# Kernel tuning notes

Hardware: AMD Instinct MI355X
Metric: run time of the kernel (lower is better)

## Reference

```python
import jax, jax.numpy as jnp
import numpy as np

N = 10000
H_INPUTS = 128
H = 512
RW_LEN = 16
BATCH = 512


def setup_inputs() -> dict:
    key = jax.random.key(0)
    ks = jax.random.split(key, 5)
    x = jax.random.normal(ks[0], (BATCH, RW_LEN, N + 1), dtype=jnp.float32)
    # xavier-ish scaled params
    W_down = jax.random.normal(ks[1], (N, H_INPUTS), dtype=jnp.float32) * (1.0 / np.sqrt(N))
    W_cell = jax.random.normal(ks[2], (H_INPUTS + 1 + H, 4 * H), dtype=jnp.float32) * (1.0 / np.sqrt(H_INPUTS + 1 + H))
    b_cell = jnp.zeros((4 * H,), dtype=jnp.float32)
    W_out = jax.random.normal(ks[3], (H, 1), dtype=jnp.float32) * (1.0 / np.sqrt(H))
    b_out = jnp.zeros((1,), dtype=jnp.float32)
    return {"x": x, "W_down": W_down, "W_cell": W_cell, "b_cell": b_cell,
            "W_out": W_out, "b_out": b_out}


def _forward(x, W_down, W_cell, b_cell, W_out, b_out):
    B = x.shape[0]
    x_rw = x[:, :, :N]                       # [B, T, N]
    x_weights = x[:, :, -1:]                 # [B, T, 1]
    xa = jnp.einsum('btn,nh->bth', x_rw, W_down)  # down-projection [B, T, H_in]
    xc = jnp.concatenate([xa, x_weights], axis=2)  # [B, T, H_in+1]
    xc_t = jnp.swapaxes(xc, 0, 1)            # [T, B, H_in+1] for scan

    h0 = jnp.zeros((B, H), dtype=x.dtype)
    c0 = jnp.zeros((B, H), dtype=x.dtype)

    def step(carry, xt):
        h, c = carry
        gates = jnp.concatenate([xt, h], axis=1) @ W_cell + b_cell  # [B, 4H]
        i_g, c_g, f_g, o_g = jnp.split(gates, 4, axis=1)
        # custom forget-gate bias of +1
        c_new = c * jax.nn.sigmoid(f_g + 1.0) + jax.nn.sigmoid(i_g) * jnp.tanh(c_g)
        h_new = jax.nn.sigmoid(o_g) * jnp.tanh(c_new)
        return (h_new, c_new), None

    (h, _), _ = jax.lax.scan(step, (h0, c0), xc_t)
    pred = h @ W_out + b_out                 # [B, 1]
    return pred


def reference(x, W_down, W_cell, b_cell, W_out, b_out):
    return _forward(x, W_down, W_cell, b_cell, W_out, b_out)
```

## Files before the change

kernel.cpp:

```cpp
#include <hip/hip_runtime.h>
#include <cmath>

#define TID ((int)threadIdx.x)

typedef __bf16 bf16_t;
typedef bf16_t bf16x8 __attribute__((ext_vector_type(8)));
typedef float floatx4 __attribute__((ext_vector_type(4)));

#define MFMA(a, b, c) __builtin_amdgcn_mfma_f32_16x16x32_bf16(a, b, c, 0, 0, 0)
#define WAIT_BAR(N)  do { asm volatile("s_waitcnt vmcnt(" #N ")" ::: "memory"); \
                          __builtin_amdgcn_s_barrier(); \
                          __builtin_amdgcn_sched_barrier(0); } while (0)
#define LGKM_BAR     do { asm volatile("s_waitcnt lgkmcnt(0)" ::: "memory"); \
                          __builtin_amdgcn_s_barrier(); \
                          __builtin_amdgcn_sched_barrier(0); } while (0)

constexpr int N_IN = 10000;
constexpr int XP   = 10001;
constexpr int KPD  = 10240;
constexpr int HH   = 512;
constexpr int TT   = 16;
constexpr int NB   = 512;
constexpr int MROW = 8192;
constexpr int KSPLIT = 16;
constexpr int KCHUNK = 640;
constexpr int KT_A = 10;

__device__ __forceinline__ float sigm(float x) { return 1.0f / (1.0f + expf(-x)); }

__device__ __forceinline__ void gload16(const void* g, void* lds) {
  __builtin_amdgcn_global_load_lds(
      (const __attribute__((address_space(1))) unsigned int*)g,
      (__attribute__((address_space(3))) unsigned int*)lds, 16, 0, 0);
}

__global__ __launch_bounds__(256)
void kPrepWd(const float* __restrict__ Wd, bf16_t* __restrict__ Whi, bf16_t* __restrict__ Wlo) {
  __shared__ float Ts[64][133];
  const int k0 = blockIdx.x * 64;
  #pragma unroll
  for (int i = 0; i < 32; ++i) {
    int f = TID + 256 * i;
    int kk = f >> 7, c = f & 127;
    int k = k0 + kk;
    Ts[kk][c] = (k < N_IN) ? Wd[(size_t)k * 128 + c] : 0.0f;
  }
  __syncthreads();
  const int lane = TID & 63, w = TID >> 6;
  for (int pass = 0; pass < 32; ++pass) {
    int c = pass * 4 + w;
    float v = Ts[lane][c];
    bf16_t hi = (bf16_t)v;
    bf16_t lo = (bf16_t)(v - (float)hi);
    Whi[(size_t)c * KPD + k0 + lane] = hi;
    Wlo[(size_t)c * KPD + k0 + lane] = lo;
  }
}

__global__ __launch_bounds__(256)
void kPrepWc(const float* __restrict__ Wc, bf16_t* __restrict__ Wxh, bf16_t* __restrict__ Wxl,
             float* __restrict__ wN, bf16_t* __restrict__ Whh, bf16_t* __restrict__ Whl) {
  __shared__ float Ts[64][133];
  const int k0 = blockIdx.x * 64;
  const int c0 = blockIdx.y * 128;
  #pragma unroll
  for (int i = 0; i < 32; ++i) {
    int f = TID + 256 * i;
    int kk = f >> 7, cc = f & 127;
    int k = k0 + kk;
    Ts[kk][cc] = (k < 641) ? Wc[(size_t)k * 2048 + c0 + cc] : 0.0f;
  }
  __syncthreads();
  const int lane = TID & 63, w = TID >> 6;
  const int k = k0 + lane;
  for (int pass = 0; pass < 32; ++pass) {
    int cc = pass * 4 + w;
    int c = c0 + cc;
    float v = Ts[lane][cc];
    bf16_t hi = (bf16_t)v;
    bf16_t lo = (bf16_t)(v - (float)hi);
    if (k < 128) {
      Wxh[(size_t)c * 128 + k] = hi;
      Wxl[(size_t)c * 128 + k] = lo;
    } else if (k == 128) {
      wN[c] = v;
    } else if (k < 641) {
      Whh[(size_t)c * 512 + (k - 129)] = hi;
      Whl[(size_t)c * 512 + (k - 129)] = lo;
    }
  }
}

__global__ __launch_bounds__(256, 2)
void kA_mfma(const float* __restrict__ x, const bf16_t* __restrict__ Whi,
             const bf16_t* __restrict__ Wlo, float* __restrict__ parts) {
  __shared__ __align__(16) bf16_t Bt[2][2048 * 8];
  const int lane = TID & 63, w = TID >> 6;
  const int row0 = blockIdx.x * 128 + w * 32;
  const int kbase = blockIdx.y * KCHUNK;
  floatx4 acc[2][8] = {};

  auto STAGE = [&](int buf, int kt) {
    const int k0 = kbase + kt * 64;
    #pragma unroll
    for (int i = 0; i < 8; ++i) {
      int L = i * 256 + TID;
      int arr = L >> 10, col = (L >> 3) & 127, g = L & 7;
      int gs = g ^ (col & 7);
      const bf16_t* src = (arr ? Wlo : Whi) + (size_t)col * KPD + k0 + gs * 8;
      gload16(src, &Bt[buf][(size_t)L * 8]);
    }
  };
  auto LOADX = [&](float4 (&xb)[2][2][2], int kt) {
    const int k0 = kbase + kt * 64;
    #pragma unroll
    for (int rf = 0; rf < 2; ++rf) {
      const float* xp = x + (size_t)(row0 + rf * 16 + (lane & 15)) * XP;
      #pragma unroll
      for (int h = 0; h < 2; ++h) {
        int kk0 = k0 + h * 32 + (lane >> 4) * 8;
        int kc = (kk0 < N_IN) ? kk0 : (N_IN - 8);
        float4 v0 = *(const float4*)(xp + kc);
        float4 v1 = *(const float4*)(xp + kc + 4);
        if (kk0 >= N_IN) {
          v0 = make_float4(0.f, 0.f, 0.f, 0.f);
          v1 = make_float4(0.f, 0.f, 0.f, 0.f);
        }
        xb[rf][h][0] = v0;
        xb[rf][h][1] = v1;
      }
    }
  };
  auto COMPUTE = [&](int buf, const float4 (&xb)[2][2][2]) {
    #pragma unroll
    for (int h = 0; h < 2; ++h) {
      const int p = h * 4 + (lane >> 4);
      bf16x8 ahi[2], alo[2];
      #pragma unroll
      for (int rf = 0; rf < 2; ++rf) {
        float vv[8] = {xb[rf][h][0].x, xb[rf][h][0].y, xb[rf][h][0].z, xb[rf][h][0].w,
                       xb[rf][h][1].x, xb[rf][h][1].y, xb[rf][h][1].z, xb[rf][h][1].w};
        #pragma unroll
        for (int e = 0; e < 8; ++e) {
          bf16_t hi = (bf16_t)vv[e];
          ahi[rf][e] = hi;
          alo[rf][e] = (bf16_t)(vv[e] - (float)hi);
        }
      }
      #pragma unroll
      for (int cf = 0; cf < 8; ++cf) {
        const int col = cf * 16 + (lane & 15);
        const int g = p ^ (col & 7);
        bf16x8 bhi = *(const bf16x8*)&Bt[buf][(col * 8 + g) * 8];
        bf16x8 blo = *(const bf16x8*)&Bt[buf][(1024 + col * 8 + g) * 8];
        #pragma unroll
        for (int rf = 0; rf < 2; ++rf) {
          acc[rf][cf] = MFMA(ahi[rf], bhi, acc[rf][cf]);
          acc[rf][cf] = MFMA(ahi[rf], blo, acc[rf][cf]);
          acc[rf][cf] = MFMA(alo[rf], bhi, acc[rf][cf]);
        }
      }
    }
  };

  float4 xb0[2][2][2], xb1[2][2][2], xb2[2][2][2];
  STAGE(0, 0); LOADX(xb0, 0);
  STAGE(1, 1); LOADX(xb1, 1);
  LOADX(xb2, 2);
  #pragma unroll
  for (int kt = 0; kt < KT_A; ++kt) {
    if (kt <= KT_A - 3)      WAIT_BAR(24);
    else if (kt == KT_A - 2) WAIT_BAR(16);
    else                     WAIT_BAR(0);
    if (kt % 3 == 0)      COMPUTE(kt & 1, xb0);
    else if (kt % 3 == 1) COMPUTE(kt & 1, xb1);
    else                  COMPUTE(kt & 1, xb2);
    LGKM_BAR;
    if (kt + 2 < KT_A) STAGE(kt & 1, kt + 2);
    if (kt + 3 < KT_A) {
      if ((kt + 3) % 3 == 0)      LOADX(xb0, kt + 3);
      else if ((kt + 3) % 3 == 1) LOADX(xb1, kt + 3);
      else                        LOADX(xb2, kt + 3);
    }
  }

  float* dst = parts + (size_t)blockIdx.y * MROW * 128;
  #pragma unroll
  for (int rf = 0; rf < 2; ++rf)
    #pragma unroll
    for (int cf = 0; cf < 8; ++cf)
      #pragma unroll
      for (int r = 0; r < 4; ++r) {
        int row = row0 + rf * 16 + (lane >> 4) * 4 + r;
        int col = cf * 16 + (lane & 15);
        dst[(size_t)row * 128 + col] = acc[rf][cf][r];
      }
}

__global__ __launch_bounds__(256)
void kRed(const float* __restrict__ parts, float* __restrict__ xa) {
  size_t i4 = ((size_t)blockIdx.x * 256 + TID) * 4;
  float4 v = make_float4(0.f, 0.f, 0.f, 0.f);
  #pragma unroll
  for (int s = 0; s < KSPLIT; ++s) {
    float4 p = *(const float4*)&parts[(size_t)s * MROW * 128 + i4];
    v.x += p.x; v.y += p.y; v.z += p.z; v.w += p.w;
  }
  *(float4*)&xa[i4] = v;
}

__global__ __launch_bounds__(512, 2)
void kGx(const float* __restrict__ xa, const float* __restrict__ x,
         const bf16_t* __restrict__ Wxh, const bf16_t* __restrict__ Wxl,
         const float* __restrict__ wN, const float* __restrict__ bc,
         float* __restrict__ gx) {
  __shared__ __align__(16) bf16_t Bt[4096 * 8];
  const int lane = TID & 63, w = TID >> 6;
  const int wr = w & 3, wc = w >> 2;
  const int rowbase = blockIdx.x * 128 + wr * 32;
  const int JB = blockIdx.y * 32;
  floatx4 acc[2][4] = {};

  #pragma unroll
  for (int i = 0; i < 8; ++i) {
    int L = i * 512 + TID;
    int arr = L >> 11, ce = (L >> 4) & 127, g = L & 15;
    int gs = g ^ (ce & 15);
    int c_src = (ce & 3) * 512 + JB + (ce >> 2);
    const bf16_t* src = (arr ? Wxl : Wxh) + (size_t)c_src * 128 + gs * 8;
    gload16(src, &Bt[(size_t)L * 8]);
  }
  float4 xb[2][2][2][2];
  #pragma unroll
  for (int kt = 0; kt < 2; ++kt)
    #pragma unroll
    for (int rf = 0; rf < 2; ++rf) {
      const float* ap = xa + (size_t)(rowbase + rf * 16 + (lane & 15)) * 128;
      #pragma unroll
      for (int h = 0; h < 2; ++h) {
        int kk0 = kt * 64 + h * 32 + (lane >> 4) * 8;
        xb[kt][rf][h][0] = *(const float4*)(ap + kk0);
        xb[kt][rf][h][1] = *(const float4*)(ap + kk0 + 4);
      }
    }
  __syncthreads();
  #pragma unroll
  for (int kt = 0; kt < 2; ++kt) {
    #pragma unroll
    for (int h = 0; h < 2; ++h) {
      const int p = kt * 8 + h * 4 + (lane >> 4);
      bf16x8 ahi[2], alo[2];
      #pragma unroll
      for (int rf = 0; rf < 2; ++rf) {
        float vv[8] = {xb[kt][rf][h][0].x, xb[kt][rf][h][0].y, xb[kt][rf][h][0].z, xb[kt][rf][h][0].w,
                       xb[kt][rf][h][1].x, xb[kt][rf][h][1].y, xb[kt][rf][h][1].z, xb[kt][rf][h][1].w};
        #pragma unroll
        for (int e = 0; e < 8; ++e) {
          bf16_t hi = (bf16_t)vv[e];
          ahi[rf][e] = hi;
          alo[rf][e] = (bf16_t)(vv[e] - (float)hi);
        }
      }
      #pragma unroll
      for (int cf = 0; cf < 4; ++cf) {
        const int ce = wc * 64 + cf * 16 + (lane & 15);
        const int g = p ^ (ce & 15);
        bf16x8 bhi = *(const bf16x8*)&Bt[(ce * 16 + g) * 8];
        bf16x8 blo = *(const bf16x8*)&Bt[(2048 + ce * 16 + g) * 8];
        #pragma unroll
        for (int rf = 0; rf < 2; ++rf) {
          acc[rf][cf] = MFMA(ahi[rf], bhi, acc[rf][cf]);
          acc[rf][cf] = MFMA(ahi[rf], blo, acc[rf][cf]);
          acc[rf][cf] = MFMA(alo[rf], bhi, acc[rf][cf]);
        }
      }
    }
  }
  #pragma unroll
  for (int rf = 0; rf < 2; ++rf)
    #pragma unroll
    for (int cf = 0; cf < 4; ++cf) {
      const int ce = wc * 64 + cf * 16 + (lane & 15);
      const int n = blockIdx.y * 128 + ce;
      const int c_src = (ce & 3) * 512 + JB + (ce >> 2);
      const float bias = bc[c_src];
      const float wn = wN[c_src];
      #pragma unroll
      for (int r = 0; r < 4; ++r) {
        int row = rowbase + rf * 16 + (lane >> 4) * 4 + r;
        float xwv = x[(size_t)row * XP + N_IN];
        gx[(size_t)row * 2048 + n] = acc[rf][cf][r] + bias + xwv * wn;
      }
    }
}

__global__ __launch_bounds__(128, 2)
void kStepH(const bf16_t* __restrict__ hhi_in, const bf16_t* __restrict__ hlo_in,
            const bf16_t* __restrict__ Whh, const bf16_t* __restrict__ Whl,
            const float* __restrict__ gx, const float* __restrict__ c_in,
            bf16_t* __restrict__ hhi_out, bf16_t* __restrict__ hlo_out,
            float* __restrict__ c_out, int t, int has_h) {
  __shared__ __align__(16) bf16_t Bt[2][1024 * 8];
  const int lane = TID & 63, w = TID >> 6;
  const int j0 = blockIdx.x * 16;
  const int brow0 = blockIdx.y * 32 + w * 16;
  floatx4 acc[4] = {};

  auto STAGE = [&](int buf, int kt) {
    const int k0 = kt * 64;
    #pragma unroll
    for (int i = 0; i < 8; ++i) {
      int L = i * 128 + TID;
      int arr = L >> 9, ce = (L >> 3) & 63, g = L & 7;
      int gs = g ^ (ce & 7);
      int c_src = (ce >> 4) * 512 + j0 + (ce & 15);
      const bf16_t* src = (arr ? Whl : Whh) + (size_t)c_src * 512 + k0 + gs * 8;
      gload16(src, &Bt[buf][(size_t)L * 8]);
    }
  };
  auto LOADA = [&](bf16x8 (&ar)[2][2], int kt) {
    const int b = brow0 + (lane & 15);
    #pragma unroll
    for (int h = 0; h < 2; ++h) {
      const int kk0 = kt * 64 + h * 32 + (lane >> 4) * 8;
      ar[h][0] = *(const bf16x8*)&hhi_in[(size_t)b * HH + kk0];
      ar[h][1] = *(const bf16x8*)&hlo_in[(size_t)b * HH + kk0];
    }
  };
  auto COMPUTE = [&](int buf, const bf16x8 (&ar)[2][2]) {
    #pragma unroll
    for (int h = 0; h < 2; ++h) {
      const int p = h * 4 + (lane >> 4);
      #pragma unroll
      for (int cf = 0; cf < 4; ++cf) {
        const int ce = cf * 16 + (lane & 15);
        const int g = p ^ (ce & 7);
        bf16x8 bhi = *(const bf16x8*)&Bt[buf][(ce * 8 + g) * 8];
        bf16x8 blo = *(const bf16x8*)&Bt[buf][(512 + ce * 8 + g) * 8];
        acc[cf] = MFMA(ar[h][0], bhi, acc[cf]);
        acc[cf] = MFMA(ar[h][0], blo, acc[cf]);
        acc[cf] = MFMA(ar[h][1], bhi, acc[cf]);
      }
    }
  };

  if (has_h) {
    bf16x8 aA[2][2], aB[2][2];
    STAGE(0, 0);
    LOADA(aA, 0);
    #pragma unroll
    for (int kt = 0; kt < 8; kt += 2) {
      if (kt + 1 < 8) {
        STAGE(1, kt + 1); LOADA(aB, kt + 1);
        WAIT_BAR(12);
      } else {
        WAIT_BAR(0);
      }
      COMPUTE(0, aA);
      LGKM_BAR;
      if (kt + 2 < 8) {
        STAGE(0, kt + 2); LOADA(aA, kt + 2);
        WAIT_BAR(12);
      } else {
        WAIT_BAR(0);
      }
      COMPUTE(1, aB);
      LGKM_BAR;
    }
  }

  const int j = j0 + (lane & 15);
  #pragma unroll
  for (int r = 0; r < 4; ++r) {
    int b = brow0 + (lane >> 4) * 4 + r;
    float4 gv = *(const float4*)&gx[((size_t)b * TT + t) * 2048 + (size_t)j * 4];
    float gi = acc[0][r] + gv.x;
    float gc = acc[1][r] + gv.y;
    float gf = acc[2][r] + gv.z;
    float go = acc[3][r] + gv.w;
    float cp = has_h ? c_in[(size_t)b * HH + j] : 0.0f;
    float cn = cp * sigm(gf + 1.0f) + sigm(gi) * tanhf(gc);
    float hn = sigm(go) * tanhf(cn);
    c_out[(size_t)b * HH + j] = cn;
    bf16_t hh = (bf16_t)hn;
    hhi_out[(size_t)b * HH + j] = hh;
    hlo_out[(size_t)b * HH + j] = (bf16_t)(hn - (float)hh);
  }
}

__global__ __launch_bounds__(64)
void kC_out(const bf16_t* __restrict__ hh, const bf16_t* __restrict__ hl,
            const float* __restrict__ Wo, const float* __restrict__ bo,
            float* __restrict__ out) {
  const int b = blockIdx.x;
  float s = 0.0f;
  for (int j = TID; j < HH; j += 64)
    s += ((float)hh[(size_t)b * HH + j] + (float)hl[(size_t)b * HH + j]) * Wo[j];
  #pragma unroll
  for (int off = 32; off > 0; off >>= 1) s += __shfl_down(s, off);
  if (TID == 0) out[b] = s + bo[0];
}

extern "C" void kernel_launch(void* const* d_in, const int* in_sizes, int n_in,
                              void* d_out, int out_size, void* d_ws, size_t ws_size,
                              hipStream_t stream) {
  const float* x  = (const float*)d_in[0];
  const float* Wd = (const float*)d_in[1];
  const float* Wc = (const float*)d_in[2];
  const float* bc = (const float*)d_in[3];
  const float* Wo = (const float*)d_in[4];
  const float* bo = (const float*)d_in[5];
  float* out = (float*)d_out;

  char* wsb = (char*)d_ws;
  size_t off = 0;
  auto alloc = [&](size_t bytes) -> void* {
    void* p = wsb + off;
    off = (off + bytes + 255) & ~(size_t)255;
    return p;
  };
  bf16_t* WdThi = (bf16_t*)alloc((size_t)128 * KPD * 2);
  bf16_t* WdTlo = (bf16_t*)alloc((size_t)128 * KPD * 2);
  bf16_t* WxThi = (bf16_t*)alloc((size_t)2048 * 128 * 2);
  bf16_t* WxTlo = (bf16_t*)alloc((size_t)2048 * 128 * 2);
  bf16_t* WhThi = (bf16_t*)alloc((size_t)2048 * 512 * 2);
  bf16_t* WhTlo = (bf16_t*)alloc((size_t)2048 * 512 * 2);
  float*  wN    = (float*)alloc(2048 * 4);
  float*  xa    = (float*)alloc((size_t)MROW * 128 * 4);
  float*  parts = (float*)alloc((size_t)KSPLIT * MROW * 128 * 4);
  float*  gx    = parts;
  bf16_t* h0hi = (bf16_t*)alloc((size_t)NB * HH * 2);
  bf16_t* h0lo = (bf16_t*)alloc((size_t)NB * HH * 2);
  bf16_t* h1hi = (bf16_t*)alloc((size_t)NB * HH * 2);
  bf16_t* h1lo = (bf16_t*)alloc((size_t)NB * HH * 2);
  float*  c0   = (float*)alloc((size_t)NB * HH * 4);
  float*  c1   = (float*)alloc((size_t)NB * HH * 4);
  bf16_t* hhi[2] = {h0hi, h1hi};
  bf16_t* hlo[2] = {h0lo, h1lo};
  float*  cb[2]  = {c0, c1};

  kPrepWd<<<160, 256, 0, stream>>>(Wd, WdThi, WdTlo);
  kPrepWc<<<dim3(11, 16), 256, 0, stream>>>(Wc, WxThi, WxTlo, wN, WhThi, WhTlo);
  kA_mfma<<<dim3(64, KSPLIT), 256, 0, stream>>>(x, WdThi, WdTlo, parts);
  kRed<<<1024, 256, 0, stream>>>(parts, xa);
  kGx<<<dim3(64, 16), 512, 0, stream>>>(xa, x, WxThi, WxTlo, wN, bc, gx);
  for (int t = 0; t < TT; ++t) {
    kStepH<<<dim3(32, 16), 128, 0, stream>>>(hhi[t & 1], hlo[t & 1], WhThi, WhTlo,
        gx, cb[t & 1], hhi[(t + 1) & 1], hlo[(t + 1) & 1], cb[(t + 1) & 1],
        t, (t == 0) ? 0 : 1);
  }
  kC_out<<<512, 64, 0, stream>>>(h0hi, h0lo, Wo, bo, out);
}
```

Before: 402.0 us.

## Fuse 16 LSTM step launches into one persistent kernel with grid barrier

Replaces the 16 per-timestep kStepH launches with a single persistent kernel that loops over timesteps and synchronises all 512 blocks through a global atomic counter barrier. This removes per-launch overhead and the tail/ramp between dependent step kernels. It relies on all 512 blocks being co-resident (launch bounds 128,2 over 256 CUs), otherwise it would deadlock. The spin barrier also adds atomic traffic and fence latency at every step.

```diff
diff --git a/kernel.cpp b/kernel.cpp
--- a/kernel.cpp
+++ b/kernel.cpp
@@ -25,6 +25,7 @@
 constexpr int KSPLIT = 16;
 constexpr int KCHUNK = 640;
 constexpr int KT_A = 10;
+constexpr int NBLK_STEPS = 512;
 
 __device__ __forceinline__ float sigm(float x) { return 1.0f / (1.0f + expf(-x)); }
 
@@ -295,16 +296,20 @@
 }
 
 __global__ __launch_bounds__(128, 2)
-void kStepH(const bf16_t* __restrict__ hhi_in, const bf16_t* __restrict__ hlo_in,
-            const bf16_t* __restrict__ Whh, const bf16_t* __restrict__ Whl,
-            const float* __restrict__ gx, const float* __restrict__ c_in,
-            bf16_t* __restrict__ hhi_out, bf16_t* __restrict__ hlo_out,
-            float* __restrict__ c_out, int t, int has_h) {
+void kStepsP(const bf16_t* __restrict__ Whh, const bf16_t* __restrict__ Whl,
+             const float* __restrict__ gx,
+             bf16_t* __restrict__ h0hi, bf16_t* __restrict__ h0lo,
+             bf16_t* __restrict__ h1hi, bf16_t* __restrict__ h1lo,
+             float* __restrict__ c0, float* __restrict__ c1,
+             unsigned* __restrict__ bar) {
   __shared__ __align__(16) bf16_t Bt[2][1024 * 8];
   const int lane = TID & 63, w = TID >> 6;
   const int j0 = blockIdx.x * 16;
   const int brow0 = blockIdx.y * 32 + w * 16;
-  floatx4 acc[4] = {};
+
+  bf16_t* hhi[2] = {h0hi, h1hi};
+  bf16_t* hlo[2] = {h0lo, h1lo};
+  float*  cb[2]  = {c0, c1};
 
   auto STAGE = [&](int buf, int kt) {
     const int k0 = kt * 64;
@@ -318,16 +323,7 @@
       gload16(src, &Bt[buf][(size_t)L * 8]);
     }
   };
-  auto LOADA = [&](bf16x8 (&ar)[2][2], int kt) {
-    const int b = brow0 + (lane & 15);
-    #pragma unroll
-    for (int h = 0; h < 2; ++h) {
-      const int kk0 = kt * 64 + h * 32 + (lane >> 4) * 8;
-      ar[h][0] = *(const bf16x8*)&hhi_in[(size_t)b * HH + kk0];
-      ar[h][1] = *(const bf16x8*)&hlo_in[(size_t)b * HH + kk0];
-    }
-  };
-  auto COMPUTE = [&](int buf, const bf16x8 (&ar)[2][2]) {
+  auto COMPUTE = [&](int buf, const bf16x8 (&ar)[2][2], floatx4 (&acc)[4]) {
     #pragma unroll
     for (int h = 0; h < 2; ++h) {
       const int p = h * 4 + (lane >> 4);
@@ -344,47 +340,76 @@
     }
   };
 
-  if (has_h) {
-    bf16x8 aA[2][2], aB[2][2];
-    STAGE(0, 0);
-    LOADA(aA, 0);
-    #pragma unroll
-    for (int kt = 0; kt < 8; kt += 2) {
-      if (kt + 1 < 8) {
-        STAGE(1, kt + 1); LOADA(aB, kt + 1);
-        WAIT_BAR(12);
-      } else {
-        WAIT_BAR(0);
-      }
-      COMPUTE(0, aA);
-      LGKM_BAR;
-      if (kt + 2 < 8) {
-        STAGE(0, kt + 2); LOADA(aA, kt + 2);
-        WAIT_BAR(12);
-      } else {
-        WAIT_BAR(0);
-      }
-      COMPUTE(1, aB);
-      LGKM_BAR;
-    }
-  }
-
-  const int j = j0 + (lane & 15);
-  #pragma unroll
-  for (int r = 0; r < 4; ++r) {
-    int b = brow0 + (lane >> 4) * 4 + r;
-    float4 gv = *(const float4*)&gx[((size_t)b * TT + t) * 2048 + (size_t)j * 4];
-    float gi = acc[0][r] + gv.x;
-    float gc = acc[1][r] + gv.y;
-    float gf = acc[2][r] + gv.z;
-    float go = acc[3][r] + gv.w;
-    float cp = has_h ? c_in[(size_t)b * HH + j] : 0.0f;
-    float cn = cp * sigm(gf + 1.0f) + sigm(gi) * tanhf(gc);
-    float hn = sigm(go) * tanhf(cn);
-    c_out[(size_t)b * HH + j] = cn;
-    bf16_t hh = (bf16_t)hn;
-    hhi_out[(size_t)b * HH + j] = hh;
-    hlo_out[(size_t)b * HH + j] = (bf16_t)(hn - (float)hh);
+  #pragma unroll 1
+  for (int t = 0; t < TT; ++t) {
+    floatx4 acc[4] = {};
+    if (t > 0) {
+      __syncthreads();
+      if (TID == 0) {
+        __threadfence();
+        __hip_atomic_fetch_add(bar, 1u, __ATOMIC_ACQ_REL, __HIP_MEMORY_SCOPE_AGENT);
+        const unsigned target = (unsigned)t * NBLK_STEPS;
+        while (__hip_atomic_load(bar, __ATOMIC_ACQUIRE, __HIP_MEMORY_SCOPE_AGENT) < target) {
+          __builtin_amdgcn_s_sleep(4);
+        }
+        __threadfence();
+      }
+      __syncthreads();
+      const bf16_t* hi_in = hhi[t & 1];
+      const bf16_t* lo_in = hlo[t & 1];
+      auto LOADA = [&](bf16x8 (&ar)[2][2], int kt) {
+        const int b = brow0 + (lane & 15);
+        #pragma unroll
+        for (int h = 0; h < 2; ++h) {
+          const int kk0 = kt * 64 + h * 32 + (lane >> 4) * 8;
+          ar[h][0] = *(const bf16x8*)&hi_in[(size_t)b * HH + kk0];
+          ar[h][1] = *(const bf16x8*)&lo_in[(size_t)b * HH + kk0];
+        }
+      };
+      bf16x8 aA[2][2], aB[2][2];
+      STAGE(0, 0);
+      LOADA(aA, 0);
+      #pragma unroll
+      for (int kt = 0; kt < 8; kt += 2) {
+        if (kt + 1 < 8) {
+          STAGE(1, kt + 1); LOADA(aB, kt + 1);
+          WAIT_BAR(12);
+        } else {
+          WAIT_BAR(0);
+        }
+        COMPUTE(0, aA, acc);
+        LGKM_BAR;
+        if (kt + 2 < 8) {
+          STAGE(0, kt + 2); LOADA(aA, kt + 2);
+          WAIT_BAR(12);
+        } else {
+          WAIT_BAR(0);
+        }
+        COMPUTE(1, aB, acc);
+        LGKM_BAR;
+      }
+    }
+    const int j = j0 + (lane & 15);
+    const float* cin = cb[t & 1];
+    float* cout = cb[(t + 1) & 1];
+    bf16_t* hho = hhi[(t + 1) & 1];
+    bf16_t* hlo_o = hlo[(t + 1) & 1];
+    #pragma unroll
+    for (int r = 0; r < 4; ++r) {
+      int b = brow0 + (lane >> 4) * 4 + r;
+      float4 gv = *(const float4*)&gx[((size_t)b * TT + t) * 2048 + (size_t)j * 4];
+      float gi = acc[0][r] + gv.x;
+      float gc = acc[1][r] + gv.y;
+      float gf = acc[2][r] + gv.z;
+      float go = acc[3][r] + gv.w;
+      float cp = (t > 0) ? cin[(size_t)b * HH + j] : 0.0f;
+      float cn = cp * sigm(gf + 1.0f) + sigm(gi) * tanhf(gc);
+      float hn = sigm(go) * tanhf(cn);
+      cout[(size_t)b * HH + j] = cn;
+      bf16_t hh = (bf16_t)hn;
+      hho[(size_t)b * HH + j] = hh;
+      hlo_o[(size_t)b * HH + j] = (bf16_t)(hn - (float)hh);
+    }
   }
 }
 
@@ -435,19 +460,15 @@
   bf16_t* h1lo = (bf16_t*)alloc((size_t)NB * HH * 2);
   float*  c0   = (float*)alloc((size_t)NB * HH * 4);
   float*  c1   = (float*)alloc((size_t)NB * HH * 4);
-  bf16_t* hhi[2] = {h0hi, h1hi};
-  bf16_t* hlo[2] = {h0lo, h1lo};
-  float*  cb[2]  = {c0, c1};
-
+  unsigned* bar = (unsigned*)alloc(256);
+
+  hipMemsetAsync(bar, 0, 256, stream);
   kPrepWd<<<160, 256, 0, stream>>>(Wd, WdThi, WdTlo);
   kPrepWc<<<dim3(11, 16), 256, 0, stream>>>(Wc, WxThi, WxTlo, wN, WhThi, WhTlo);
   kA_mfma<<<dim3(64, KSPLIT), 256, 0, stream>>>(x, WdThi, WdTlo, parts);
   kRed<<<1024, 256, 0, stream>>>(parts, xa);
   kGx<<<dim3(64, 16), 512, 0, stream>>>(xa, x, WxThi, WxTlo, wN, bc, gx);
-  for (int t = 0; t < TT; ++t) {
-    kStepH<<<dim3(32, 16), 128, 0, stream>>>(hhi[t & 1], hlo[t & 1], WhThi, WhTlo,
-        gx, cb[t & 1], hhi[(t + 1) & 1], hlo[(t + 1) & 1], cb[(t + 1) & 1],
-        t, (t == 0) ? 0 : 1);
-  }
+  kStepsP<<<dim3(32, 16), 128, 0, stream>>>(WhThi, WhTlo, gx,
+      h0hi, h0lo, h1hi, h1lo, c0, c1, bar);
   kC_out<<<512, 64, 0, stream>>>(h0hi, h0lo, Wo, bo, out);
 }
```

Measured after the change: 1.304 ms. 3.25x slower.
